# Kernel tuning notes

Measured on AMD Instinct MI355X. Metric: run time of the kernel, lower is better.

Reference implementation:

```python
import jax, jax.numpy as jnp
import numpy as np

B, T, D = 2, 2048, 2048
H, HD = 16, 128          # num heads, head dim (H*HD == D)
F = 8192                 # SwiGLU intermediate size
EPS = 1e-6               # RMSNorm eps
THETA = 10000.0          # RoPE base


def rms_norm(x, w):
    var = jnp.mean(x * x, axis=-1, keepdims=True)
    return x * jax.lax.rsqrt(var + EPS) * w


def rotate_half(x):
    x1, x2 = jnp.split(x, 2, axis=-1)
    return jnp.concatenate([-x2, x1], axis=-1)


def setup_inputs() -> dict:
    key = jax.random.key(0)
    ks = jax.random.split(key, 24)
    s = 0.02
    p = lambda i, shape: (s * jax.random.normal(ks[i], shape)).astype(jnp.float32)
    return {
        "hidden_states": jax.random.normal(ks[0], (B, T, D), dtype=jnp.float32),
        # Qwen2 attention (q/k/v have bias, o does not)
        "q_w": p(1, (D, H * HD)), "q_b": p(2, (H * HD,)),
        "k_w": p(3, (D, H * HD)), "k_b": p(4, (H * HD,)),
        "v_w": p(5, (D, H * HD)), "v_b": p(6, (H * HD,)),
        "o_w": p(7, (H * HD, D)),
        "ln1_w": jnp.ones((D,), jnp.float32),
        "ln2_w": jnp.ones((D,), jnp.float32),
        # SwiGLU MLP
        "gate_w": p(8, (D, F)), "up_w": p(9, (D, F)), "down_w": p(10, (F, D)),
        # transition network (2-layer SiLU MLP predicting the residual)
        "t1_w": p(11, (D, D)), "t1_b": jnp.zeros((D,), jnp.float32),
        "t2_w": p(12, (D, D)), "t2_b": jnp.zeros((D,), jnp.float32),
        # causal router: per-token scalar logit
        "r_w": p(13, (D, 1)), "r_b": jnp.zeros((1,), jnp.float32),
    }


def reference(hidden_states, q_w, q_b, k_w, k_b, v_w, v_b, o_w, ln1_w, ln2_w,
              gate_w, up_w, down_w, t1_w, t1_b, t2_w, t2_b, r_w, r_b):
    Bc, Tc, Dc = hidden_states.shape
    x_original = hidden_states

    # ---- Qwen2 decoder block ----
    h = rms_norm(hidden_states, ln1_w)
    q = (h @ q_w + q_b).reshape(Bc, Tc, H, HD).transpose(0, 2, 1, 3)
    k = (h @ k_w + k_b).reshape(Bc, Tc, H, HD).transpose(0, 2, 1, 3)
    v = (h @ v_w + v_b).reshape(Bc, Tc, H, HD).transpose(0, 2, 1, 3)

    # RoPE
    inv_freq = 1.0 / (THETA ** (jnp.arange(0, HD, 2, dtype=jnp.float32) / HD))
    freqs = jnp.arange(Tc, dtype=jnp.float32)[:, None] * inv_freq[None, :]
    emb = jnp.concatenate([freqs, freqs], axis=-1)          # [T, HD]
    cos = jnp.cos(emb)[None, None]
    sin = jnp.sin(emb)[None, None]
    q = q * cos + rotate_half(q) * sin
    k = k * cos + rotate_half(k) * sin

    scores = jnp.einsum("bhqd,bhkd->bhqk", q, k) / jnp.sqrt(jnp.float32(HD))
    causal = jnp.tril(jnp.ones((Tc, Tc), dtype=bool))
    scores = jnp.where(causal[None, None], scores, jnp.float32(-1e9))
    attn = jax.nn.softmax(scores, axis=-1)
    ctx = jnp.einsum("bhqk,bhkd->bhqd", attn, v)
    ctx = ctx.transpose(0, 2, 1, 3).reshape(Bc, Tc, H * HD)
    x = hidden_states + ctx @ o_w

    h2 = rms_norm(x, ln2_w)
    mlp = (jax.nn.silu(h2 @ gate_w) * (h2 @ up_w)) @ down_w
    x_posterior = x + mlp

    # ---- TPN: predict residual from shifted posterior states ----
    actual_residual = x_posterior - x_original
    prev = jnp.concatenate(
        [jnp.zeros((Bc, 1, Dc), x_posterior.dtype), x_posterior[:, :-1, :]], axis=1)
    predicted_residual = jax.nn.silu(prev @ t1_w + t1_b) @ t2_w + t2_b
    tpn_loss = jnp.mean(
        (predicted_residual - jax.lax.stop_gradient(actual_residual)) ** 2)

    # ---- predictive router (teacher): surprise-based gate + binary targets ----
    err = jnp.mean((actual_residual - predicted_residual) ** 2, axis=-1)  # [B,T]
    g_continuous = jax.nn.sigmoid(
        (err - jnp.mean(err)) / (jnp.std(err) + 1e-6))
    binary_targets = (g_continuous > 0.5).astype(jnp.float32)

    # ---- causal router (student) + BCE-with-logits against detached targets ----
    causal_scores = (x_original @ r_w + r_b)[..., 0]                      # [B,T]
    causal_probs = jax.nn.sigmoid(causal_scores)
    t = jax.lax.stop_gradient(binary_targets)
    s = causal_scores
    causal_loss = jnp.mean(
        jnp.maximum(s, 0.0) - s * t + jnp.log1p(jnp.exp(-jnp.abs(s))))

    return (x_posterior, tpn_loss, causal_loss, g_continuous,
            binary_targets, causal_probs)
```

## Files before the change

kernel.cpp:

```cpp
#include <hip/hip_runtime.h>
#include <math.h>

#define B_SZ 2
#define T_SEQ 2048
#define D_MODEL 2048
#define NHEAD 16
#define HDIM 128
#define FFN 8192
#define NTOK (B_SZ*T_SEQ)

#define OFF_TPN 8388608
#define OFF_CL  8388609
#define OFF_G   8388610
#define OFF_B   8392706
#define OFF_CP  8396802

#define RLO 1024.0f
#define RLOI 9.765625e-4f

typedef __attribute__((ext_vector_type(8))) _Float16 f16x8;
typedef __attribute__((ext_vector_type(4))) float f32x4;
typedef unsigned int u32;
typedef const u32 __attribute__((address_space(1)))* gas_p;
typedef u32 __attribute__((address_space(3)))* las_p;

__device__ __forceinline__ void gload16(const _Float16* g, _Float16* l) {
  __builtin_amdgcn_global_load_lds((gas_p)g, (las_p)l, 16, 0, 0);
}
__device__ __forceinline__ f16x8 ld8h(const _Float16* p) {
  return *reinterpret_cast<const f16x8*>(p);
}
__device__ __forceinline__ f32x4 mfma16h(f16x8 a, f16x8 b, f32x4 c) {
  return __builtin_amdgcn_mfma_f32_16x16x32_f16(a, b, c, 0, 0, 0);
}
__device__ __forceinline__ f32x4 zero4() { f32x4 z = {0.f,0.f,0.f,0.f}; return z; }
__device__ __forceinline__ float wredsum(float v) {
  #pragma unroll
  for (int d = 1; d < 64; d <<= 1) v += __shfl_xor(v, d, 64);
  return v;
}
__device__ __forceinline__ void split1(float v, _Float16& h, _Float16& l) {
  _Float16 hh = (_Float16)v;
  h = hh;
  l = (_Float16)((v - (float)hh) * RLO);
}

__global__ __launch_bounds__(256) void wsplit_kernel(const float* __restrict__ src,
                                                     _Float16* __restrict__ dhi,
                                                     _Float16* __restrict__ dlo,
                                                     int srcStride, int r0, int c0,
                                                     int R) {
  __shared__ float tile[32][33];
  int cb = blockIdx.x * 32, rb = blockIdx.y * 32;
  int tx = threadIdx.x, ty = threadIdx.y;
  #pragma unroll
  for (int i = 0; i < 4; ++i)
    tile[ty + i*8][tx] = src[(size_t)(r0 + rb + ty + i*8) * srcStride + c0 + cb + tx];
  __syncthreads();
  #pragma unroll
  for (int i = 0; i < 4; ++i) {
    float v = tile[tx][ty + i*8];
    _Float16 h, l; split1(v, h, l);
    size_t idx = (size_t)(cb + ty + i*8) * R + rb + tx;
    dhi[idx] = h; dlo[idx] = l;
  }
}

__global__ __launch_bounds__(256) void rmsnorm_kernel(const float* __restrict__ x,
                                                      const float* __restrict__ wgt,
                                                      _Float16* __restrict__ oh,
                                                      _Float16* __restrict__ ol) {
  const int row = blockIdx.x, tid = threadIdx.x;
  const float* xr = x + (size_t)row * D_MODEL;
  float4 v0 = *(const float4*)(xr + tid*8);
  float4 v1 = *(const float4*)(xr + tid*8 + 4);
  float ss = v0.x*v0.x + v0.y*v0.y + v0.z*v0.z + v0.w*v0.w
           + v1.x*v1.x + v1.y*v1.y + v1.z*v1.z + v1.w*v1.w;
  ss = wredsum(ss);
  __shared__ float red[4];
  if ((tid & 63) == 0) red[tid >> 6] = ss;
  __syncthreads();
  float tot = red[0] + red[1] + red[2] + red[3];
  float inv = 1.f / sqrtf(tot / (float)D_MODEL + 1e-6f);
  float4 w0 = *(const float4*)(wgt + tid*8);
  float4 w1 = *(const float4*)(wgt + tid*8 + 4);
  float f[8];
  f[0]=v0.x*inv*w0.x; f[1]=v0.y*inv*w0.y; f[2]=v0.z*inv*w0.z; f[3]=v0.w*inv*w0.w;
  f[4]=v1.x*inv*w1.x; f[5]=v1.y*inv*w1.y; f[6]=v1.z*inv*w1.z; f[7]=v1.w*inv*w1.w;
  f16x8 hh, ll;
  #pragma unroll
  for (int i = 0; i < 8; ++i) { _Float16 h, l; split1(f[i], h, l); hh[i]=h; ll[i]=l; }
  *(f16x8*)(oh + (size_t)row * D_MODEL + tid*8) = hh;
  *(f16x8*)(ol + (size_t)row * D_MODEL + tid*8) = ll;
}

template<int MODE, bool OUT_SPLIT, bool QKV>
__global__ __launch_bounds__(256) void gemm2_kernel(
    const _Float16* __restrict__ Ahi, const _Float16* __restrict__ Alo,
    const _Float16* __restrict__ Bhi, const _Float16* __restrict__ Blo,
    const float* __restrict__ b0, const float* __restrict__ b1,
    const float* __restrict__ b2, const float* __restrict__ resid,
    const _Float16* __restrict__ ghi, const _Float16* __restrict__ glo,
    void* __restrict__ C1, void* __restrict__ C2,
    int M, int N, int K) {
  const int nbn = gridDim.x, nbm = gridDim.y;
  int bid = blockIdx.y * nbn + blockIdx.x;
  bid = (bid & 7) * ((nbn * nbm) >> 3) + (bid >> 3);
  const int nig = nbn << 3;
  const int gid = bid / nig, rem = bid - gid * nig;
  const int by = (gid << 3) + (rem & 7);
  const int bx = rem >> 3;
  int sel = 0;
  const float* bias = b0;
  size_t cbase = 0, bwoff = 0;
  if (QKV) {
    sel = blockIdx.z;
    bias = (sel == 0) ? b0 : ((sel == 1) ? b1 : b2);
    bwoff = (size_t)sel * D_MODEL * D_MODEL;
    cbase = (size_t)sel * (size_t)NTOK * D_MODEL;
  }
  const int n0 = bx * 128, m0 = by * 128;
  const int tid = threadIdx.x, lane = tid & 63, wv = tid >> 6;
  const int wr = wv >> 1, wc = wv & 1;
  const int l16 = lane & 15, lg = lane >> 4;
  __shared__ _Float16 SH[2 * 4 * 128 * 32];
  f32x4 acc1[4][4], acc2[4][4];
  #pragma unroll
  for (int i = 0; i < 4; ++i)
    #pragma unroll
    for (int j = 0; j < 4; ++j) { acc1[i][j] = zero4(); acc2[i][j] = zero4(); }
  const int srow = wv * 32 + (lane >> 2);
  const int scol = ((lane & 3) ^ ((lane >> 2) & 3)) * 8;
  const _Float16* ga0  = Ahi + (size_t)(m0 + srow) * K + scol;
  const _Float16* ga1  = ga0 + (size_t)16 * K;
  const _Float16* gal0 = Alo + (size_t)(m0 + srow) * K + scol;
  const _Float16* gal1 = gal0 + (size_t)16 * K;
  const _Float16* gb0  = Bhi + bwoff + (size_t)(n0 + srow) * K + scol;
  const _Float16* gb1  = gb0 + (size_t)16 * K;
  const _Float16* gbl0 = Blo + bwoff + (size_t)(n0 + srow) * K + scol;
  const _Float16* gbl1 = gbl0 + (size_t)16 * K;
  const int dbase = wv * 32 * 32;
  const int csw = (lg ^ (l16 & 3)) * 8;

  #define STAGE(buf, kk) do {                                   \
    _Float16* sb = SH + (buf) * 16384;                          \
    gload16(ga0  + (kk), sb          + dbase);                  \
    gload16(ga1  + (kk), sb          + dbase + 512);            \
    gload16(gal0 + (kk), sb + 4096  + dbase);                   \
    gload16(gal1 + (kk), sb + 4096  + dbase + 512);             \
    gload16(gb0  + (kk), sb + 8192  + dbase);                   \
    gload16(gb1  + (kk), sb + 8192  + dbase + 512);             \
    gload16(gbl0 + (kk), sb + 12288 + dbase);                   \
    gload16(gbl1 + (kk), sb + 12288 + dbase + 512);             \
  } while (0)

  int cur = 0;
  STAGE(0, 0);
  __syncthreads();
  for (int kk = 0; kk < K; kk += 32) {
    if (kk + 32 < K) STAGE(cur ^ 1, kk + 32);
    const _Float16* sb = SH + cur * 16384;
    f16x8 af_h[4], af_l[4];
    #pragma unroll
    for (int i = 0; i < 4; ++i) {
      const int off = (wr*64 + i*16 + l16) * 32 + csw;
      af_h[i] = ld8h(sb + off);
      af_l[i] = ld8h(sb + 4096 + off);
    }
    #pragma unroll
    for (int j = 0; j < 4; ++j) {
      const int offb = (wc*64 + j*16 + l16) * 32 + csw;
      f16x8 bh = ld8h(sb + 8192 + offb);
      f16x8 bl = ld8h(sb + 12288 + offb);
      #pragma unroll
      for (int i = 0; i < 4; ++i) {
        acc1[i][j] = mfma16h(af_h[i], bh, acc1[i][j]);
        acc2[i][j] = mfma16h(af_h[i], bl, acc2[i][j]);
        acc2[i][j] = mfma16h(af_l[i], bh, acc2[i][j]);
      }
    }
    __syncthreads();
    cur ^= 1;
  }
  #undef STAGE
  #pragma unroll
  for (int i = 0; i < 4; ++i) {
    const int row0 = m0 + wr*64 + i*16 + lg*4;
    #pragma unroll
    for (int j = 0; j < 4; ++j) {
      const int col = n0 + wc*64 + j*16 + l16;
      float bv = (MODE == 1 || MODE == 2) ? bias[col] : 0.f;
      #pragma unroll
      for (int t = 0; t < 4; ++t) {
        const int row = row0 + t;
        size_t idx;
        if (QKV && sel == 2)
          idx = cbase + (size_t)(row >> 11) * ((size_t)D_MODEL * T_SEQ)
                      + (size_t)col * T_SEQ + (row & (T_SEQ - 1));
        else
          idx = cbase + (size_t)row * N + col;
        float v = acc1[i][j][t] + acc2[i][j][t] * RLOI + bv;
        if (MODE == 2) v = v / (1.f + expf(-v));
        if (MODE == 3) v += resid[idx];
        if (MODE == 4) {
          float g = (float)ghi[idx] + (float)glo[idx] * RLOI;
          v = g / (1.f + expf(-g)) * v;
        }
        if (OUT_SPLIT) {
          _Float16 h, l; split1(v, h, l);
          ((_Float16*)C1)[idx] = h;
          ((_Float16*)C2)[idx] = l;
        } else {
          ((float*)C1)[idx] = v;
        }
      }
    }
  }
}

__global__ __launch_bounds__(256) void rope_kernel(_Float16* __restrict__ Qh,
                                                   _Float16* __restrict__ Ql,
                                                   _Float16* __restrict__ Kh,
                                                   _Float16* __restrict__ Kl) {
  const int row = blockIdx.x;
  const int tpos = row & (T_SEQ - 1);
  __shared__ float svs[64], cvs[64];
  if (threadIdx.x < 64) {
    double invf = exp(-(double)threadIdx.x * (9.210340371976184 / 64.0));
    double ph = fmod((double)tpos * invf, 6.283185307179586476925);
    sincosf((float)ph, &svs[threadIdx.x], &cvs[threadIdx.x]);
  }
  __syncthreads();
  for (int item = threadIdx.x; item < NHEAD * 64; item += 256) {
    const int h = item >> 6, d = item & 63;
    const float sv = svs[d], cv = cvs[d];
    const size_t i0 = (size_t)row * D_MODEL + h*HDIM + d;
    const size_t i1 = i0 + 64;
    float q0 = (float)Qh[i0] + (float)Ql[i0]*RLOI;
    float q1 = (float)Qh[i1] + (float)Ql[i1]*RLOI;
    float k0 = (float)Kh[i0] + (float)Kl[i0]*RLOI;
    float k1 = (float)Kh[i1] + (float)Kl[i1]*RLOI;
    _Float16 hh, ll;
    split1(q0*cv - q1*sv, hh, ll); Qh[i0]=hh; Ql[i0]=ll;
    split1(q1*cv + q0*sv, hh, ll); Qh[i1]=hh; Ql[i1]=ll;
    split1(k0*cv - k1*sv, hh, ll); Kh[i0]=hh; Kl[i0]=ll;
    split1(k1*cv + k0*sv, hh, ll); Kh[i1]=hh; Kl[i1]=ll;
  }
}

__global__ __launch_bounds__(256) void attn_kernel(
    const _Float16* __restrict__ Qh, const _Float16* __restrict__ Ql,
    const _Float16* __restrict__ Kh, const _Float16* __restrict__ Kl,
    const _Float16* __restrict__ VTh, const _Float16* __restrict__ VTl,
    _Float16* __restrict__ Oh, _Float16* __restrict__ Ol) {
  const int qb = (int)gridDim.x - 1 - (int)blockIdx.x;
  const int bhid = blockIdx.y;
  const int b = bhid >> 4, h = bhid & 15;
  const int tid = threadIdx.x, lane = tid & 63, w = tid >> 6;
  const int l16 = lane & 15, lg = lane >> 4;
  __shared__ _Float16 Ksh[32][128], Ksl[32][128];
  __shared__ _Float16 Vth[128][32], Vtl[128][32];
  __shared__ _Float16 Psh[4][16][40], Psl[4][16][40];
  const size_t hbase  = (size_t)b * T_SEQ * D_MODEL + (size_t)h * HDIM;
  const size_t vtbase = (size_t)bhid * (size_t)HDIM * T_SEQ;
  const size_t qrow0 = (size_t)qb * 64;

  f16x8 qf_h[4], qf_l[4];
  {
    const size_t qoff = hbase + (qrow0 + w*16 + l16) * D_MODEL + lg*8;
    #pragma unroll
    for (int c = 0; c < 4; ++c) {
      qf_h[c] = ld8h(Qh + qoff + c*32);
      qf_l[c] = ld8h(Ql + qoff + c*32);
    }
  }
  f32x4 acc1[8], acc2[8];
  #pragma unroll
  for (int df = 0; df < 8; ++df) { acc1[df] = zero4(); acc2[df] = zero4(); }
  float mrow[4] = {-3e38f,-3e38f,-3e38f,-3e38f};
  float drow[4] = {0.f,0.f,0.f,0.f};

  const int krow = w*8 + (lane >> 4);
  const int kch0 = ((lane & 15) ^ (krow & 7)) * 8;
  const int kch1 = ((lane & 15) ^ ((krow + 4) & 7)) * 8;
  const _Float16* gkh0 = Kh + hbase + (size_t)krow * D_MODEL + kch0;
  const _Float16* gkh1 = Kh + hbase + (size_t)(krow + 4) * D_MODEL + kch1;
  const _Float16* gkl0 = Kl + hbase + (size_t)krow * D_MODEL + kch0;
  const _Float16* gkl1 = Kl + hbase + (size_t)(krow + 4) * D_MODEL + kch1;
  _Float16* dkh0 = &Ksh[w*8][0];   _Float16* dkh1 = &Ksh[w*8+4][0];
  _Float16* dkl0 = &Ksl[w*8][0];   _Float16* dkl1 = &Ksl[w*8+4][0];
  const int vrow = w*32 + (lane >> 2);
  const int vcol = (lane & 3) * 8;
  const _Float16* gvh0 = VTh + vtbase + (size_t)vrow * T_SEQ + vcol;
  const _Float16* gvh1 = gvh0 + (size_t)16 * T_SEQ;
  const _Float16* gvl0 = VTl + vtbase + (size_t)vrow * T_SEQ + vcol;
  const _Float16* gvl1 = gvl0 + (size_t)16 * T_SEQ;
  _Float16* dvh0 = &Vth[w*32][0];  _Float16* dvh1 = &Vth[w*32+16][0];
  _Float16* dvl0 = &Vtl[w*32][0];  _Float16* dvl1 = &Vtl[w*32+16][0];

  const int nkb = (qb + 1) * 2;
  const float scale = 0.088388347648318447f;

  for (int kb = 0; kb < nkb; ++kb) {
    __syncthreads();
    const size_t ko = (size_t)kb * 32 * D_MODEL;
    const size_t vo = (size_t)kb * 32;
    gload16(gkh0 + ko, dkh0);  gload16(gkh1 + ko, dkh1);
    gload16(gkl0 + ko, dkl0);  gload16(gkl1 + ko, dkl1);
    gload16(gvh0 + vo, dvh0);  gload16(gvh1 + vo, dvh1);
    gload16(gvl0 + vo, dvl0);  gload16(gvl1 + vo, dvl1);
    __syncthreads();

    f32x4 s0 = zero4(), s0x = zero4(), s1 = zero4(), s1x = zero4();
    #pragma unroll
    for (int c = 0; c < 4; ++c) {
      const int pk = ((4*c + lg) ^ (l16 & 7)) * 8;
      f16x8 kh0 = ld8h(&Ksh[l16][pk]);
      f16x8 kl0 = ld8h(&Ksl[l16][pk]);
      f16x8 kh1 = ld8h(&Ksh[16 + l16][pk]);
      f16x8 kl1 = ld8h(&Ksl[16 + l16][pk]);
      s0  = mfma16h(qf_h[c], kh0, s0);
      s0x = mfma16h(qf_h[c], kl0, s0x);
      s0x = mfma16h(qf_l[c], kh0, s0x);
      s1  = mfma16h(qf_h[c], kh1, s1);
      s1x = mfma16h(qf_h[c], kl1, s1x);
      s1x = mfma16h(qf_l[c], kh1, s1x);
    }

    float p0[4], p1[4], corrv[4];
    #pragma unroll
    for (int t = 0; t < 4; ++t) {
      int qrow = qb*64 + w*16 + lg*4 + t;
      float a  = (s0[t] + s0x[t] * RLOI) * scale;
      float bb = (s1[t] + s1x[t] * RLOI) * scale;
      if (kb*32      + l16 > qrow) a  = -1e9f;
      if (kb*32 + 16 + l16 > qrow) bb = -1e9f;
      float mx = fmaxf(a, bb);
      #pragma unroll
      for (int d = 1; d < 16; d <<= 1) mx = fmaxf(mx, __shfl_xor(mx, d, 64));
      float mnew = fmaxf(mrow[t], mx);
      float corr = expf(mrow[t] - mnew);
      float e0 = expf(a - mnew), e1 = expf(bb - mnew);
      float ps = e0 + e1;
      #pragma unroll
      for (int d = 1; d < 16; d <<= 1) ps += __shfl_xor(ps, d, 64);
      drow[t] = drow[t] * corr + ps;
      mrow[t] = mnew;
      corrv[t] = corr;
      p0[t] = e0; p1[t] = e1;
    }
    #pragma unroll
    for (int df = 0; df < 8; ++df)
      #pragma unroll
      for (int t = 0; t < 4; ++t) { acc1[df][t] *= corrv[t]; acc2[df][t] *= corrv[t]; }

    #pragma unroll
    for (int t = 0; t < 4; ++t) {
      _Float16 hh, ll;
      split1(p0[t], hh, ll);
      Psh[w][lg*4 + t][l16] = hh;  Psl[w][lg*4 + t][l16] = ll;
      split1(p1[t], hh, ll);
      Psh[w][lg*4 + t][16 + l16] = hh;  Psl[w][lg*4 + t][16 + l16] = ll;
    }
    asm volatile("s_waitcnt lgkmcnt(0)" ::: "memory");
    __builtin_amdgcn_sched_barrier(0);
    f16x8 pf_h = ld8h(&Psh[w][l16][lg*8]);
    f16x8 pf_l = ld8h(&Psl[w][l16][lg*8]);
    #pragma unroll
    for (int df = 0; df < 8; ++df) {
      f16x8 vh = ld8h(&Vth[df*16 + l16][lg*8]);
      f16x8 vl = ld8h(&Vtl[df*16 + l16][lg*8]);
      acc1[df] = mfma16h(pf_h, vh, acc1[df]);
      acc2[df] = mfma16h(pf_h, vl, acc2[df]);
      acc2[df] = mfma16h(pf_l, vh, acc2[df]);
    }
  }
  #pragma unroll
  for (int df = 0; df < 8; ++df)
    #pragma unroll
    for (int t = 0; t < 4; ++t) {
      float o = (acc1[df][t] + acc2[df][t] * RLOI) / drow[t];
      _Float16 hh, ll; split1(o, hh, ll);
      const size_t oo = hbase + (qrow0 + w*16 + lg*4 + t) * D_MODEL + df*16 + l16;
      Oh[oo] = hh; Ol[oo] = ll;
    }
}

__global__ __launch_bounds__(256) void shiftprev_kernel(const float* __restrict__ xpost,
                                                        _Float16* __restrict__ ph,
                                                        _Float16* __restrict__ pl) {
  const int row = blockIdx.x;
  const int tpos = row & (T_SEQ - 1);
  const size_t o = (size_t)row * D_MODEL + threadIdx.x * 8;
  f16x8 hh, ll;
  if (tpos == 0) {
    #pragma unroll
    for (int i = 0; i < 8; ++i) { hh[i] = (_Float16)0.f; ll[i] = (_Float16)0.f; }
  } else {
    const float* src = xpost + o - D_MODEL;
    #pragma unroll
    for (int i = 0; i < 8; ++i) {
      _Float16 h, l; split1(src[i], h, l); hh[i] = h; ll[i] = l;
    }
  }
  *(f16x8*)(ph + o) = hh;
  *(f16x8*)(pl + o) = ll;
}

__global__ __launch_bounds__(256) void err_kernel(const float* __restrict__ pred,
                                                  const float* __restrict__ xpost,
                                                  const float* __restrict__ xorig,
                                                  float* __restrict__ err) {
  const int row = blockIdx.x, tid = threadIdx.x;
  const size_t base = (size_t)row * D_MODEL + tid * 8;
  const float* pp = pred + base;
  const float* ap = xpost + base;
  const float* op = xorig + base;
  float ss = 0.f;
  #pragma unroll
  for (int i = 0; i < 8; ++i) {
    float d = pp[i] - (ap[i] - op[i]);
    ss += d * d;
  }
  ss = wredsum(ss);
  __shared__ float red[4];
  if ((tid & 63) == 0) red[tid >> 6] = ss;
  __syncthreads();
  if (tid == 0) err[row] = (red[0]+red[1]+red[2]+red[3]) / (float)D_MODEL;
}

__global__ __launch_bounds__(1024) void stats_kernel(const float* __restrict__ err,
                                                     float* __restrict__ dout) {
  __shared__ float red[16];
  __shared__ float sh[2];
  const int tid = threadIdx.x;
  float s = 0.f;
  for (int i = tid; i < NTOK; i += 1024) s += err[i];
  s = wredsum(s);
  if ((tid & 63) == 0) red[tid >> 6] = s;
  __syncthreads();
  if (tid == 0) {
    float t = 0.f;
    for (int i = 0; i < 16; ++i) t += red[i];
    sh[0] = t / (float)NTOK;
  }
  __syncthreads();
  const float mean = sh[0];
  float v = 0.f;
  for (int i = tid; i < NTOK; i += 1024) { float d = err[i] - mean; v += d * d; }
  v = wredsum(v);
  __syncthreads();
  if ((tid & 63) == 0) red[tid >> 6] = v;
  __syncthreads();
  if (tid == 0) {
    float t = 0.f;
    for (int i = 0; i < 16; ++i) t += red[i];
    sh[1] = sqrtf(t / (float)NTOK);
    dout[OFF_TPN] = mean;
  }
  __syncthreads();
  const float stdv = sh[1];
  for (int i = tid; i < NTOK; i += 1024) {
    float z = (err[i] - mean) / (stdv + 1e-6f);
    dout[OFF_G + i] = 1.f / (1.f + expf(-z));
    dout[OFF_B + i] = (err[i] > mean) ? 1.f : 0.f;
  }
}

__global__ __launch_bounds__(256) void cscore_kernel(const float* __restrict__ x,
                                                     const float* __restrict__ rwv,
                                                     const float* __restrict__ rbv,
                                                     float* __restrict__ cs,
                                                     float* __restrict__ probs) {
  const int row = blockIdx.x, tid = threadIdx.x;
  const float* xr = x + (size_t)row * D_MODEL + tid * 8;
  const float* wr = rwv + tid * 8;
  float s = 0.f;
  #pragma unroll
  for (int i = 0; i < 8; ++i) s += xr[i] * wr[i];
  s = wredsum(s);
  __shared__ float red[4];
  if ((tid & 63) == 0) red[tid >> 6] = s;
  __syncthreads();
  if (tid == 0) {
    float v = red[0]+red[1]+red[2]+red[3] + rbv[0];
    cs[row] = v;
    probs[row] = 1.f / (1.f + expf(-v));
  }
}

__global__ __launch_bounds__(1024) void closs_kernel(const float* __restrict__ cs,
                                                     const float* __restrict__ tgt,
                                                     float* __restrict__ outv) {
  __shared__ float red[16];
  const int tid = threadIdx.x;
  float a = 0.f;
  for (int i = tid; i < NTOK; i += 1024) {
    float s = cs[i], t = tgt[i];
    a += fmaxf(s, 0.f) - s * t + log1pf(expf(-fabsf(s)));
  }
  a = wredsum(a);
  if ((tid & 63) == 0) red[tid >> 6] = a;
  __syncthreads();
  if (tid == 0) {
    float t = 0.f;
    for (int i = 0; i < 16; ++i) t += red[i];
    outv[0] = t / (float)NTOK;
  }
}

extern "C" void kernel_launch(void* const* d_in, const int* in_sizes, int n_in,
                              void* d_out, int out_size, void* d_ws, size_t ws_size,
                              hipStream_t stream) {
  (void)in_sizes; (void)n_in; (void)out_size; (void)ws_size;
  const float* x_in = (const float*)d_in[0];
  const float* q_w  = (const float*)d_in[1];
  const float* q_b  = (const float*)d_in[2];
  const float* k_w  = (const float*)d_in[3];
  const float* k_b  = (const float*)d_in[4];
  const float* v_w  = (const float*)d_in[5];
  const float* v_b  = (const float*)d_in[6];
  const float* o_w  = (const float*)d_in[7];
  const float* ln1  = (const float*)d_in[8];
  const float* ln2  = (const float*)d_in[9];
  const float* gw   = (const float*)d_in[10];
  const float* uw   = (const float*)d_in[11];
  const float* dw   = (const float*)d_in[12];
  const float* t1w  = (const float*)d_in[13];
  const float* t1b  = (const float*)d_in[14];
  const float* t2w  = (const float*)d_in[15];
  const float* t2b  = (const float*)d_in[16];
  const float* rw   = (const float*)d_in[17];
  const float* rb   = (const float*)d_in[18];
  float* out = (float*)d_out;
  char* ws = (char*)d_ws;

  _Float16* WQKVh = (_Float16*)(ws + 0);
  _Float16* WQKVl = (_Float16*)(ws + 25165824);
  _Float16* WOh   = (_Float16*)(ws + 0);
  _Float16* WOl   = (_Float16*)(ws + 8388608);
  _Float16* WDh   = (_Float16*)(ws + 0);
  _Float16* WDl   = (_Float16*)(ws + 16777216);
  _Float16* WT1h  = (_Float16*)(ws + 0);
  _Float16* WT1l  = (_Float16*)(ws + 8388608);
  _Float16* WT2h  = (_Float16*)(ws + 16777216);
  _Float16* WT2l  = (_Float16*)(ws + 25165824);
  _Float16* Hh    = (_Float16*)(ws + 50331648);
  _Float16* Hl    = (_Float16*)(ws + 67108864);
  _Float16* PREVh = Hh;
  _Float16* PREVl = Hl;
  _Float16* QKVh  = (_Float16*)(ws + 83886080);
  _Float16* QKVl  = (_Float16*)(ws + 134217728);
  _Float16* CTXh  = (_Float16*)(ws + 184549376);
  _Float16* CTXl  = (_Float16*)(ws + 201326592);
  _Float16* WGh   = (_Float16*)(ws + 83886080);
  _Float16* WGl   = (_Float16*)(ws + 100663296);
  _Float16* WUh   = (_Float16*)(ws + 117440512);
  _Float16* WUl   = (_Float16*)(ws + 134217728);
  _Float16* MLPh  = (_Float16*)(ws + 150994944);
  _Float16* MLPl  = (_Float16*)(ws + 184549376);
  _Float16* A1h   = (_Float16*)(ws + 83886080);
  _Float16* A1l   = (_Float16*)(ws + 100663296);
  float*    PREDf = (float*)   (ws + 117440512);
  float*    ERRf  = (float*)   (ws + 150994944);
  float*    CSf   = (float*)   (ws + 151011328);

  const size_t DD = (size_t)D_MODEL * D_MODEL;
  const size_t TD = (size_t)NTOK * D_MODEL;
  dim3 tb(32, 8);
  const dim3 gW22(64, 64);
  const dim3 gWg(128, 64);
  const dim3 gWd(64, 128);

  wsplit_kernel<<<gW22, tb, 0, stream>>>(q_w, WQKVh,        WQKVl,        D_MODEL, 0, 0, D_MODEL);
  wsplit_kernel<<<gW22, tb, 0, stream>>>(k_w, WQKVh + DD,   WQKVl + DD,   D_MODEL, 0, 0, D_MODEL);
  wsplit_kernel<<<gW22, tb, 0, stream>>>(v_w, WQKVh + 2*DD, WQKVl + 2*DD, D_MODEL, 0, 0, D_MODEL);
  rmsnorm_kernel<<<NTOK, 256, 0, stream>>>(x_in, ln1, Hh, Hl);
  gemm2_kernel<1,true,true><<<dim3(16,32,3),256,0,stream>>>(
      Hh, Hl, WQKVh, WQKVl, q_b, k_b, v_b, nullptr, nullptr, nullptr,
      QKVh, QKVl, NTOK, D_MODEL, D_MODEL);
  rope_kernel<<<NTOK, 256, 0, stream>>>(QKVh, QKVl, QKVh + TD, QKVl + TD);
  attn_kernel<<<dim3(T_SEQ/64, B_SZ*NHEAD), 256, 0, stream>>>(
      QKVh, QKVl, QKVh + TD, QKVl + TD, QKVh + 2*TD, QKVl + 2*TD, CTXh, CTXl);
  wsplit_kernel<<<gW22, tb, 0, stream>>>(o_w, WOh, WOl, D_MODEL, 0, 0, D_MODEL);
  gemm2_kernel<3,false,false><<<dim3(16,32),256,0,stream>>>(
      CTXh, CTXl, WOh, WOl, nullptr, nullptr, nullptr, x_in, nullptr, nullptr,
      out, nullptr, NTOK, D_MODEL, D_MODEL);
  rmsnorm_kernel<<<NTOK, 256, 0, stream>>>(out, ln2, Hh, Hl);
  for (int half = 0; half < 2; ++half) {
    const int f0 = half * (FFN/2);
    wsplit_kernel<<<gWg, tb, 0, stream>>>(gw, WGh, WGl, FFN, 0, f0, D_MODEL);
    wsplit_kernel<<<gWg, tb, 0, stream>>>(uw, WUh, WUl, FFN, 0, f0, D_MODEL);
    gemm2_kernel<0,true,false><<<dim3(32,32),256,0,stream>>>(
        Hh, Hl, WGh, WGl, nullptr, nullptr, nullptr, nullptr, nullptr, nullptr,
        MLPh, MLPl, NTOK, FFN/2, D_MODEL);
    gemm2_kernel<4,true,false><<<dim3(32,32),256,0,stream>>>(
        Hh, Hl, WUh, WUl, nullptr, nullptr, nullptr, nullptr, MLPh, MLPl,
        MLPh, MLPl, NTOK, FFN/2, D_MODEL);
    wsplit_kernel<<<gWd, tb, 0, stream>>>(dw, WDh, WDl, D_MODEL, f0, 0, FFN/2);
    gemm2_kernel<3,false,false><<<dim3(16,32),256,0,stream>>>(
        MLPh, MLPl, WDh, WDl, nullptr, nullptr, nullptr, out, nullptr, nullptr,
        out, nullptr, NTOK, D_MODEL, FFN/2);
  }
  shiftprev_kernel<<<NTOK, 256, 0, stream>>>(out, PREVh, PREVl);
  wsplit_kernel<<<gW22, tb, 0, stream>>>(t1w, WT1h, WT1l, D_MODEL, 0, 0, D_MODEL);
  wsplit_kernel<<<gW22, tb, 0, stream>>>(t2w, WT2h, WT2l, D_MODEL, 0, 0, D_MODEL);
  gemm2_kernel<2,true,false><<<dim3(16,32),256,0,stream>>>(
      PREVh, PREVl, WT1h, WT1l, t1b, nullptr, nullptr, nullptr, nullptr, nullptr,
      A1h, A1l, NTOK, D_MODEL, D_MODEL);
  gemm2_kernel<1,false,false><<<dim3(16,32),256,0,stream>>>(
      A1h, A1l, WT2h, WT2l, t2b, nullptr, nullptr, nullptr, nullptr, nullptr,
      PREDf, nullptr, NTOK, D_MODEL, D_MODEL);
  err_kernel<<<NTOK, 256, 0, stream>>>(PREDf, out, x_in, ERRf);
  stats_kernel<<<1, 1024, 0, stream>>>(ERRf, out);
  cscore_kernel<<<NTOK, 256, 0, stream>>>(x_in, rw, rb, CSf, out + OFF_CP);
  closs_kernel<<<1, 1024, 0, stream>>>(CSf, out + OFF_B, out + OFF_CL);
}
```

Baseline: 3.023 ms.

## Double-buffer attention K/V tiles, load V-low directly to registers, use fast exp

The attention kernel now keeps two LDS buffers for the K and V-high tiles and prefetches the next key block while the current one is computed, so each iteration needs one barrier instead of two. The V low-part fragments are read straight from global memory into registers instead of being staged through LDS, which cuts shared-memory footprint. expf is replaced by __expf in the attention softmax and the SiLU epilogues of the GEMM. This trades extra LDS use and uncoalesced global reads for more overlap, and __expf is slightly less accurate.

```diff
diff --git a/kernel.cpp b/kernel.cpp
--- a/kernel.cpp
+++ b/kernel.cpp
@@ -200,11 +200,11 @@
         else
           idx = cbase + (size_t)row * N + col;
         float v = acc1[i][j][t] + acc2[i][j][t] * RLOI + bv;
-        if (MODE == 2) v = v / (1.f + expf(-v));
+        if (MODE == 2) v = v / (1.f + __expf(-v));
         if (MODE == 3) v += resid[idx];
         if (MODE == 4) {
           float g = (float)ghi[idx] + (float)glo[idx] * RLOI;
-          v = g / (1.f + expf(-g)) * v;
+          v = g / (1.f + __expf(-g)) * v;
         }
         if (OUT_SPLIT) {
           _Float16 h, l; split1(v, h, l);
@@ -258,8 +258,8 @@
   const int b = bhid >> 4, h = bhid & 15;
   const int tid = threadIdx.x, lane = tid & 63, w = tid >> 6;
   const int l16 = lane & 15, lg = lane >> 4;
-  __shared__ _Float16 Ksh[32][128], Ksl[32][128];
-  __shared__ _Float16 Vth[128][32], Vtl[128][32];
+  __shared__ _Float16 KS[2][2][32][128];
+  __shared__ _Float16 VSh[2][128][32];
   __shared__ _Float16 Psh[4][16][40], Psl[4][16][40];
   const size_t hbase  = (size_t)b * T_SEQ * D_MODEL + (size_t)h * HDIM;
   const size_t vtbase = (size_t)bhid * (size_t)HDIM * T_SEQ;
@@ -287,38 +287,44 @@
   const _Float16* gkh1 = Kh + hbase + (size_t)(krow + 4) * D_MODEL + kch1;
   const _Float16* gkl0 = Kl + hbase + (size_t)krow * D_MODEL + kch0;
   const _Float16* gkl1 = Kl + hbase + (size_t)(krow + 4) * D_MODEL + kch1;
-  _Float16* dkh0 = &Ksh[w*8][0];   _Float16* dkh1 = &Ksh[w*8+4][0];
-  _Float16* dkl0 = &Ksl[w*8][0];   _Float16* dkl1 = &Ksl[w*8+4][0];
   const int vrow = w*32 + (lane >> 2);
   const int vcol = (lane & 3) * 8;
   const _Float16* gvh0 = VTh + vtbase + (size_t)vrow * T_SEQ + vcol;
   const _Float16* gvh1 = gvh0 + (size_t)16 * T_SEQ;
-  const _Float16* gvl0 = VTl + vtbase + (size_t)vrow * T_SEQ + vcol;
-  const _Float16* gvl1 = gvl0 + (size_t)16 * T_SEQ;
-  _Float16* dvh0 = &Vth[w*32][0];  _Float16* dvh1 = &Vth[w*32+16][0];
-  _Float16* dvl0 = &Vtl[w*32][0];  _Float16* dvl1 = &Vtl[w*32+16][0];
 
   const int nkb = (qb + 1) * 2;
   const float scale = 0.088388347648318447f;
 
+  #define ASTAGE(buf, kb) do {                                  \
+    const size_t ko = (size_t)(kb) * 32 * D_MODEL;              \
+    const size_t vo = (size_t)(kb) * 32;                        \
+    gload16(gkh0 + ko, &KS[buf][0][w*8][0]);                    \
+    gload16(gkh1 + ko, &KS[buf][0][w*8+4][0]);                  \
+    gload16(gkl0 + ko, &KS[buf][1][w*8][0]);                    \
+    gload16(gkl1 + ko, &KS[buf][1][w*8+4][0]);                  \
+    gload16(gvh0 + vo, &VSh[buf][w*32][0]);                     \
+    gload16(gvh1 + vo, &VSh[buf][w*32+16][0]);                  \
+  } while (0)
+
+  int cur = 0;
+  ASTAGE(0, 0);
+  __syncthreads();
   for (int kb = 0; kb < nkb; ++kb) {
-    __syncthreads();
-    const size_t ko = (size_t)kb * 32 * D_MODEL;
-    const size_t vo = (size_t)kb * 32;
-    gload16(gkh0 + ko, dkh0);  gload16(gkh1 + ko, dkh1);
-    gload16(gkl0 + ko, dkl0);  gload16(gkl1 + ko, dkl1);
-    gload16(gvh0 + vo, dvh0);  gload16(gvh1 + vo, dvh1);
-    gload16(gvl0 + vo, dvl0);  gload16(gvl1 + vo, dvl1);
-    __syncthreads();
+    if (kb + 1 < nkb) ASTAGE(cur ^ 1, kb + 1);
+    f16x8 vlr[8];
+    #pragma unroll
+    for (int df = 0; df < 8; ++df)
+      vlr[df] = ld8h(VTl + vtbase + (size_t)(df*16 + l16) * T_SEQ
+                     + (size_t)kb*32 + lg*8);
 
     f32x4 s0 = zero4(), s0x = zero4(), s1 = zero4(), s1x = zero4();
     #pragma unroll
     for (int c = 0; c < 4; ++c) {
       const int pk = ((4*c + lg) ^ (l16 & 7)) * 8;
-      f16x8 kh0 = ld8h(&Ksh[l16][pk]);
-      f16x8 kl0 = ld8h(&Ksl[l16][pk]);
-      f16x8 kh1 = ld8h(&Ksh[16 + l16][pk]);
-      f16x8 kl1 = ld8h(&Ksl[16 + l16][pk]);
+      f16x8 kh0 = ld8h(&KS[cur][0][l16][pk]);
+      f16x8 kl0 = ld8h(&KS[cur][1][l16][pk]);
+      f16x8 kh1 = ld8h(&KS[cur][0][16 + l16][pk]);
+      f16x8 kl1 = ld8h(&KS[cur][1][16 + l16][pk]);
       s0  = mfma16h(qf_h[c], kh0, s0);
       s0x = mfma16h(qf_h[c], kl0, s0x);
       s0x = mfma16h(qf_l[c], kh0, s0x);
@@ -339,8 +345,8 @@
       #pragma unroll
       for (int d = 1; d < 16; d <<= 1) mx = fmaxf(mx, __shfl_xor(mx, d, 64));
       float mnew = fmaxf(mrow[t], mx);
-      float corr = expf(mrow[t] - mnew);
-      float e0 = expf(a - mnew), e1 = expf(bb - mnew);
+      float corr = __expf(mrow[t] - mnew);
+      float e0 = __expf(a - mnew), e1 = __expf(bb - mnew);
       float ps = e0 + e1;
       #pragma unroll
       for (int d = 1; d < 16; d <<= 1) ps += __shfl_xor(ps, d, 64);
@@ -368,13 +374,15 @@
     f16x8 pf_l = ld8h(&Psl[w][l16][lg*8]);
     #pragma unroll
     for (int df = 0; df < 8; ++df) {
-      f16x8 vh = ld8h(&Vth[df*16 + l16][lg*8]);
-      f16x8 vl = ld8h(&Vtl[df*16 + l16][lg*8]);
+      f16x8 vh = ld8h(&VSh[cur][df*16 + l16][lg*8]);
       acc1[df] = mfma16h(pf_h, vh, acc1[df]);
-      acc2[df] = mfma16h(pf_h, vl, acc2[df]);
+      acc2[df] = mfma16h(pf_h, vlr[df], acc2[df]);
       acc2[df] = mfma16h(pf_l, vh, acc2[df]);
     }
-  }
+    __syncthreads();
+    cur ^= 1;
+  }
+  #undef ASTAGE
   #pragma unroll
   for (int df = 0; df < 8; ++df)
     #pragma unroll
```

New measurement: 3.125 ms. 1.03x slower.
